# Kernel optimization log

Measured on AMD Instinct MI355X. Metric: run time of the kernel, lower is better.

## Reference

```python
import jax, jax.numpy as jnp
import numpy as np

NSIDE = 64
NLAT = 4 * NSIDE - 1        # 255 iso-latitude rings
NLON = 4 * NSIDE            # 256 = max pixels per ring
NPIX = 12 * NSIDE * NSIDE   # 49152 HEALPix pixels
LMAX = NLAT                 # 255
MMAX = NLON // 2 + 1        # 129
BATCH, CHAN = 8, 32


def _ring_geometry():
    # HEALPix ring scheme: ring r (0-based), 1-based i=r+1
    #  north cap i<nside: nph=4i, phi shift 0.5
    #  equatorial nside<=i<=3*nside: nph=4*nside, shift alternates {0,0.5}
    #  south cap: mirror of north cap
    nph = np.zeros(NLAT, np.int64)
    shift = np.zeros(NLAT, np.float64)
    for r in range(NLAT):
        i = r + 1
        if i < NSIDE:
            nph[r], shift[r] = 4 * i, 0.5
        elif i <= 3 * NSIDE:
            nph[r], shift[r] = 4 * NSIDE, 0.5 * ((i - NSIDE + 1) % 2)
        else:
            nph[r], shift[r] = 4 * (NLAT - r), 0.5
    offs = np.concatenate([[0], np.cumsum(nph)[:-1]])
    p = np.arange(NLON)
    mask = (p[None, :] < nph[:, None])                       # [nlat, nlon]
    idx = (offs[:, None] + p[None, :]) * mask                # padded -> 0
    phase = 2.0 * np.pi * (p[None, :] + shift[:, None]) / nph[:, None] * mask
    return idx.astype(np.int32), mask.astype(np.float32), phase.astype(np.float32)


def setup_inputs() -> dict:
    key = jax.random.key(0)
    k1, k2, k3 = jax.random.split(key, 3)
    idx, mask, phase = _ring_geometry()
    x = jax.random.normal(k1, (BATCH, CHAN, NPIX), jnp.float32)
    pct = jax.random.normal(k2, (MMAX, LMAX, NLAT), jnp.float32) * 0.1  # Legendre table stand-in
    w = jax.random.uniform(k3, (NLAT,), jnp.float32)                    # per-ring quadrature weights
    return {"x": x, "pct": pct, "w": w,
            "ring_index": jnp.asarray(idx),
            "ring_mask": jnp.asarray(mask),
            "phase": jnp.asarray(phase)}


def _healpix_rfft_real(x, ring_index, ring_mask, phase):
    # x: [..., npix] -> per-ring DFT coefficients as real pairs [..., nlat, mmax, 2]
    rings = x[..., ring_index] * ring_mask                 # [..., nlat, nlon]
    m = jnp.arange(MMAX, dtype=phase.dtype)
    ang = phase[:, :, None] * m                            # [nlat, nlon, mmax]
    fr = jnp.einsum('...kp,kpm->...km', rings, jnp.cos(ang))
    fi = -jnp.einsum('...kp,kpm->...km', rings, jnp.sin(ang))
    return jnp.stack([fr, fi], axis=-1)                    # n=2 is view_as_real axis


def reference(x, pct, w, ring_index, ring_mask, phase):
    # healpix ring rFFT, then Legendre contraction (einsum '...kmn,mlk->...lmn')
    f = _healpix_rfft_real(x, ring_index, ring_mask, phase)  # [..., nlat, mmax, 2]
    weights = pct * w                                        # [mmax, lmax, nlat]
    out = jnp.einsum('...kmn,mlk->...lmn', f, weights)       # [..., lmax, mmax, 2]
    return out
```

## Files before the change

kernel.cpp:

```cpp
#include <hip/hip_runtime.h>

#define NLAT 255
#define NLON 256
#define NPIX 49152
#define MMAX 129
#define MCS  258
#define NTBL 65
#define TROWS 264

typedef unsigned short ushort_t;
typedef __attribute__((ext_vector_type(8)))  short  bf16x8;
typedef __attribute__((ext_vector_type(4)))  short  short4v;
typedef __attribute__((ext_vector_type(16))) float  f32x16;
typedef __attribute__((ext_vector_type(4)))  float  float4v;

__device__ __forceinline__ ushort_t f2bf(float f) {
    union { float f; unsigned u; } v; v.f = f;
    unsigned r = v.u + 0x7FFFu + ((v.u >> 16) & 1u);
    return (ushort_t)(r >> 16);
}
__device__ __forceinline__ float bf2f(ushort_t h) {
    union { unsigned u; float f; } v; v.u = ((unsigned)h) << 16;
    return v.f;
}

__global__ __launch_bounds__(256) void prepK(const float* __restrict__ pct,
                                             const float* __restrict__ w,
                                             ushort_t* __restrict__ pctw) {
    const int m  = blockIdx.x;
    const int l0 = blockIdx.y * 32;
    const int t  = threadIdx.x;
    const float wk = (t < NLAT) ? w[t] : 0.f;
    for (int l = l0; l < l0 + 32; ++l) {
        float v = 0.f;
        if (l < NLAT && t < NLAT)
            v = pct[((size_t)m * NLAT + l) * NLAT + t] * wk;
        pctw[((size_t)m * 256 + l) * 256 + t] = f2bf(v);
    }
}

__global__ __launch_bounds__(256) void trigK(const float* __restrict__ phase,
                                             const float* __restrict__ mask,
                                             ushort_t* __restrict__ Ttab3) {
    const int tt  = blockIdx.x;
    const int mcs = blockIdx.y;
    const int p   = threadIdx.x;
    const int r   = (tt < 63) ? tt : (tt == 63 ? 63 : 64);
    float val = 0.f;
    if (mcs < MCS) {
        float ph = phase[r * NLON + p];
        float mk = mask[r * NLON + p];
        float fm = (float)(mcs >> 1);
        float s, c;
        __sincosf(ph * fm, &s, &c);
        val = (mcs & 1) ? (-s * mk) : (c * mk);
    }
    const int pcc = p >> 6, c = (p >> 3) & 7, j = p & 7;
    Ttab3[((((size_t)tt * 4 + pcc) * 8 + c) * TROWS + mcs) * 8 + j] = f2bf(val);
}

__global__ __launch_bounds__(256, 2) void stageA(const float* __restrict__ x,
                                                 const int* __restrict__ ring_index,
                                                 const ushort_t* __restrict__ Ttab3,
                                                 ushort_t* __restrict__ f1) {
    __shared__ __align__(16) ushort_t Rs[2][64 * 72];

    const int b0 = blockIdx.x * 64;
    const int r  = blockIdx.y;
    const int i1 = r + 1;
    const int nph = (i1 < 64) ? 4 * i1 : (i1 <= 192 ? 256 : 4 * (256 - i1));
    const int tbl = (i1 < 64) ? r : (i1 <= 192 ? (63 + (((i1 - 63) & 1) ^ 1)) : 254 - r);
    const int base = ring_index[r * NLON];
    const int nchunks = (nph + 63) >> 6;

    const int t    = threadIdx.x;
    const int lane = t & 63;
    const int wid  = t >> 6;
    const int wrow = wid >> 1, wcol = wid & 1;
    const int lg   = lane >> 5;
    const int lc   = lane & 31;

    f32x16 acc[5];
#pragma unroll
    for (int tau = 0; tau < 5; ++tau)
#pragma unroll
        for (int q = 0; q < 16; ++q) acc[tau][q] = 0.f;

    int trow[5];
#pragma unroll
    for (int tau = 0; tau < 5; ++tau) {
        int rr = tau * 64 + wcol * 32 + lc;
        trow[tau] = rr > (TROWS - 1) ? (TROWS - 1) : rr;
    }

    float4v rx[4];
    const int p0 = (t & 15) * 4;
    auto ldX = [&](int pc) {
        const bool ok = (pc + p0) < nph;
#pragma unroll
        for (int pass = 0; pass < 4; ++pass) {
            int bc = (t >> 4) + pass * 16;
            float4v v = {0.f, 0.f, 0.f, 0.f};
            if (ok) v = *(const float4v*)(x + (size_t)(b0 + bc) * NPIX + base + pc + p0);
            rx[pass] = v;
        }
    };
    auto stX = [&](ushort_t* dst) {
#pragma unroll
        for (int pass = 0; pass < 4; ++pass) {
            int bc = (t >> 4) + pass * 16;
            short4v h;
            h[0] = (short)f2bf(rx[pass][0]); h[1] = (short)f2bf(rx[pass][1]);
            h[2] = (short)f2bf(rx[pass][2]); h[3] = (short)f2bf(rx[pass][3]);
            *(short4v*)(dst + bc * 72 + p0) = h;
        }
    };

    ldX(0);
    stX(Rs[0]);
    __syncthreads();

    for (int c = 0; c < nchunks; ++c) {
        const int pc = c << 6;
        const bool more = (c + 1) < nchunks;
        const ushort_t* slab = Ttab3 + (size_t)(tbl * 4 + c) * (8 * TROWS * 8);

        bf16x8 bfr[4][5];
#pragma unroll
        for (int ks = 0; ks < 4; ++ks) {
            const ushort_t* bcol = slab + (size_t)(ks * 2 + lg) * (TROWS * 8);
#pragma unroll
            for (int tau = 0; tau < 5; ++tau)
                bfr[ks][tau] = *(const bf16x8*)(bcol + trow[tau] * 8);
        }
        if (more) ldX(pc + 64);

        const ushort_t* Rcur = Rs[c & 1];
#pragma unroll
        for (int ks = 0; ks < 4; ++ks) {
            bf16x8 a = *(const bf16x8*)(Rcur + (wrow * 32 + lc) * 72 + ks * 16 + lg * 8);
#pragma unroll
            for (int tau = 0; tau < 5; ++tau)
                acc[tau] = __builtin_amdgcn_mfma_f32_32x32x16_bf16(a, bfr[ks][tau], acc[tau], 0, 0, 0);
        }
        if (more) stX(Rs[(c + 1) & 1]);
        __syncthreads();
    }

    ushort_t* Olds = Rs[0];
#pragma unroll
    for (int tau = 0; tau < 5; ++tau) {
        __syncthreads();
        {
            const int mcsl = wcol * 32 + lc;
#pragma unroll
            for (int q = 0; q < 16; ++q) {
                int bcl = wrow * 32 + 4 * lg + (q & 3) + 8 * (q >> 2);
                Olds[mcsl * 72 + bcl] = f2bf(acc[tau][q]);
            }
        }
        __syncthreads();
        {
            int row = t >> 2;
            int mcs = tau * 64 + row;
            if (mcs < MCS) {
                int m = mcs >> 1, n = mcs & 1;
                size_t gbase = ((size_t)m * NLAT + r) * 512 + n * 256 + b0 + (t & 3) * 16;
#pragma unroll
                for (int j = 0; j < 2; ++j) {
                    bf16x8 v = *(const bf16x8*)(Olds + row * 72 + (t & 3) * 16 + j * 8);
                    *(bf16x8*)(f1 + gbase + j * 8) = v;
                }
            }
        }
    }
}

__global__ __launch_bounds__(256) void transK(const ushort_t* __restrict__ f1,
                                              ushort_t* __restrict__ f1t) {
    __shared__ __align__(16) ushort_t T[64][72];
    const int m  = blockIdx.x;
    const int k0 = blockIdx.y * 64;
    const int b0 = blockIdx.z * 64;
    const int t  = threadIdx.x;
#pragma unroll
    for (int it = 0; it < 2; ++it) {
        int id = t + it * 256;
        int kk = id >> 3, ch = id & 7;
        int k  = k0 + kk;
        bf16x8 v = {0,0,0,0,0,0,0,0};
        if (k < NLAT)
            v = *(const bf16x8*)(f1 + ((size_t)m * NLAT + k) * 512 + b0 + ch * 8);
        *(bf16x8*)(&T[kk][ch * 8]) = v;
    }
    __syncthreads();
#pragma unroll
    for (int it = 0; it < 2; ++it) {
        int id  = t + it * 256;
        int bb  = id & 63, ch8 = id >> 6;
        bf16x8 v;
#pragma unroll
        for (int j = 0; j < 8; ++j) v[j] = T[ch8 * 8 + j][bb];
        *(bf16x8*)(f1t + ((size_t)m * 512 + b0 + bb) * 256 + k0 + ch8 * 8) = v;
    }
}

__global__ __launch_bounds__(256, 2) void stageB(const ushort_t* __restrict__ f1t,
                                                 const ushort_t* __restrict__ pctw,
                                                 ushort_t* __restrict__ otmp) {
    __shared__ __align__(16) ushort_t SB[30720];
    ushort_t* As = SB;
    ushort_t* Ws = SB + 10240;
    ushort_t* Es = SB;

    const int id = blockIdx.x;
    const int m  = ((id >> 5) << 3) | (id & 7);
    if (m >= MMAX) return;
    const int sub = (id >> 3) & 3;
    const int b2t = sub * 128;

    const int t     = threadIdx.x;
    const int lane  = t & 63;
    const int wid   = t >> 6;
    const int wrow  = wid >> 1, wlcol = wid & 1;
    const int lg    = lane >> 5, lc = lane & 31;

    f32x16 acc[2][4];
#pragma unroll
    for (int i = 0; i < 2; ++i)
#pragma unroll
        for (int j = 0; j < 4; ++j)
#pragma unroll
            for (int q = 0; q < 16; ++q) acc[i][j][q] = 0.f;

    bf16x8 ra[2], rw[4];
    auto ldA = [&](int kc) {
#pragma unroll
        for (int pass = 0; pass < 2; ++pass) {
            int id2 = t + pass * 256;
            int row = id2 >> 2, ch = id2 & 3;
            ra[pass] = *(const bf16x8*)(f1t + ((size_t)m * 512 + b2t + row) * 256 + kc + ch * 8);
        }
    };
    auto ldW = [&](int kc) {
#pragma unroll
        for (int pass = 0; pass < 4; ++pass) {
            int id2 = t + pass * 256;
            int row = id2 >> 2, ch = id2 & 3;
            rw[pass] = *(const bf16x8*)(pctw + ((size_t)m * 256 + row) * 256 + kc + ch * 8);
        }
    };
    auto stA = [&](ushort_t* dst) {
#pragma unroll
        for (int pass = 0; pass < 2; ++pass) {
            int id2 = t + pass * 256;
            int row = id2 >> 2, ch = id2 & 3;
            *(bf16x8*)(dst + row * 40 + ch * 8) = ra[pass];
        }
    };
    auto stW = [&](ushort_t* dst) {
#pragma unroll
        for (int pass = 0; pass < 4; ++pass) {
            int id2 = t + pass * 256;
            int row = id2 >> 2, ch = id2 & 3;
            *(bf16x8*)(dst + row * 40 + ch * 8) = rw[pass];
        }
    };

    ldA(0); ldW(0);
    stA(As); stW(Ws);
    __syncthreads();
    int buf = 0;
    for (int kc = 0; kc < 256; kc += 32, buf ^= 1) {
        const bool more = (kc + 32) < 256;
        if (more) { ldA(kc + 32); ldW(kc + 32); }
        const ushort_t* A = As + buf * 5120;
        const ushort_t* W = Ws + buf * 10240;
#pragma unroll
        for (int ks = 0; ks < 2; ++ks) {
            const int ko = ks * 16 + lg * 8;
            bf16x8 a0 = *(const bf16x8*)(A + (wrow * 64 + lc) * 40 + ko);
            bf16x8 a1 = *(const bf16x8*)(A + (wrow * 64 + 32 + lc) * 40 + ko);
#pragma unroll
            for (int jj = 0; jj < 4; ++jj) {
                bf16x8 b = *(const bf16x8*)(W + (wlcol * 128 + jj * 32 + lc) * 40 + ko);
                acc[0][jj] = __builtin_amdgcn_mfma_f32_32x32x16_bf16(a0, b, acc[0][jj], 0, 0, 0);
                acc[1][jj] = __builtin_amdgcn_mfma_f32_32x32x16_bf16(a1, b, acc[1][jj], 0, 0, 0);
            }
        }
        if (more) { stA(As + (buf ^ 1) * 5120); stW(Ws + (buf ^ 1) * 10240); }
        __syncthreads();
    }

#pragma unroll
    for (int h = 0; h < 2; ++h) {
        if (h) __syncthreads();
        if (wlcol == h) {
#pragma unroll
            for (int i = 0; i < 2; ++i)
#pragma unroll
                for (int jj = 0; jj < 4; ++jj)
#pragma unroll
                    for (int q = 0; q < 16; ++q) {
                        int bl = wrow * 64 + i * 32 + 4 * lg + (q & 3) + 8 * (q >> 2);
                        Es[bl * 136 + jj * 32 + lc] = f2bf(acc[i][jj][q]);
                    }
        }
        __syncthreads();
#pragma unroll
        for (int it = 0; it < 8; ++it) {
            int id2 = t + it * 256;
            int row = id2 >> 4, ch = id2 & 15;
            bf16x8 v = *(const bf16x8*)(Es + row * 136 + ch * 8);
            *(bf16x8*)(otmp + (((size_t)m * 512 + b2t + row) << 8) + h * 128 + ch * 8) = v;
        }
    }
}

__global__ __launch_bounds__(256) void permuteK(const ushort_t* __restrict__ otmp,
                                                float* __restrict__ out) {
    __shared__ ushort_t L[MCS * 66];
    const int bc = blockIdx.x;
    const int l0 = blockIdx.y * 64;
    const int t  = threadIdx.x;
    const int ll = t & 63;
    const int l  = l0 + ll;
#pragma unroll 4
    for (int it = 0; it < 65; ++it) {
        int mn = (t >> 6) + it * 4;
        if (mn < MCS) {
            int mm = mn >> 1, n = mn & 1;
            ushort_t v = 0;
            if (l < NLAT)
                v = otmp[(((size_t)mm * 512 + n * 256 + bc) << 8) + l];
            L[mn * 66 + ll] = v;
        }
    }
    __syncthreads();
    for (int ll2 = 0; ll2 < 64; ++ll2) {
        int lo = l0 + ll2;
        if (lo >= NLAT) break;
        size_t rowb = ((size_t)bc * NLAT + lo) * MCS;
        out[rowb + t] = bf2f(L[t * 66 + ll2]);
        if (t < 2)
            out[rowb + 256 + t] = bf2f(L[(256 + t) * 66 + ll2]);
    }
}

extern "C" void kernel_launch(void* const* d_in, const int* in_sizes, int n_in,
                              void* d_out, int out_size, void* d_ws, size_t ws_size,
                              hipStream_t stream) {
    const float* x          = (const float*)d_in[0];
    const float* pct        = (const float*)d_in[1];
    const float* w          = (const float*)d_in[2];
    const int*   ring_index = (const int*)d_in[3];
    const float* ring_mask  = (const float*)d_in[4];
    const float* phase      = (const float*)d_in[5];
    float* out = (float*)d_out;

    char* wsb = (char*)d_ws;
    char* ob  = (char*)d_out;
    ushort_t* otmp  = (ushort_t*)wsb;
    ushort_t* f1    = (ushort_t*)(wsb + 33552384);
    ushort_t* f1t   = (ushort_t*)ob;
    ushort_t* pctw  = (ushort_t*)(ob + 33816576);
    ushort_t* Ttab3 = (ushort_t*)(ob + 50724864);

    prepK   <<<dim3(MMAX, 8),     256, 0, stream>>>(pct, w, pctw);
    trigK   <<<dim3(NTBL, TROWS), 256, 0, stream>>>(phase, ring_mask, Ttab3);
    stageA  <<<dim3(4, NLAT),     256, 0, stream>>>(x, ring_index, Ttab3, f1);
    transK  <<<dim3(MMAX, 4, 8),  256, 0, stream>>>(f1, f1t);
    stageB  <<<dim3(544),         256, 0, stream>>>(f1t, pctw, otmp);
    permuteK<<<dim3(256, 4),      256, 0, stream>>>(otmp, out);
}
```

Before: 125.4 us.

## Pre-swizzle stageB operands into MFMA fragment layout and drop LDS staging

```diff
diff --git a/kernel.cpp b/kernel.cpp
--- a/kernel.cpp
+++ b/kernel.cpp
@@ -26,16 +26,17 @@
 
 __global__ __launch_bounds__(256) void prepK(const float* __restrict__ pct,
                                              const float* __restrict__ w,
-                                             ushort_t* __restrict__ pctw) {
+                                             ushort_t* __restrict__ pctwF) {
     const int m  = blockIdx.x;
     const int l0 = blockIdx.y * 32;
     const int t  = threadIdx.x;
     const float wk = (t < NLAT) ? w[t] : 0.f;
+    const int kg = t >> 3, j = t & 7;
     for (int l = l0; l < l0 + 32; ++l) {
         float v = 0.f;
         if (l < NLAT && t < NLAT)
             v = pct[((size_t)m * NLAT + l) * NLAT + t] * wk;
-        pctw[((size_t)m * 256 + l) * 256 + t] = f2bf(v);
+        pctwF[(((size_t)m * 32 + kg) * 256 + l) * 8 + j] = f2bf(v);
     }
 }
 
@@ -177,7 +178,7 @@
 }
 
 __global__ __launch_bounds__(256) void transK(const ushort_t* __restrict__ f1,
-                                              ushort_t* __restrict__ f1t) {
+                                              ushort_t* __restrict__ f1tF) {
     __shared__ __align__(16) ushort_t T[64][72];
     const int m  = blockIdx.x;
     const int k0 = blockIdx.y * 64;
@@ -201,23 +202,17 @@
         bf16x8 v;
 #pragma unroll
         for (int j = 0; j < 8; ++j) v[j] = T[ch8 * 8 + j][bb];
-        *(bf16x8*)(f1t + ((size_t)m * 512 + b0 + bb) * 256 + k0 + ch8 * 8) = v;
-    }
-}
-
-__global__ __launch_bounds__(256, 2) void stageB(const ushort_t* __restrict__ f1t,
-                                                 const ushort_t* __restrict__ pctw,
+        *(bf16x8*)(f1tF + (((size_t)m * 32 + (k0 >> 3) + ch8) * 512 + b0 + bb) * 8) = v;
+    }
+}
+
+__global__ __launch_bounds__(256, 2) void stageB(const ushort_t* __restrict__ f1tF,
+                                                 const ushort_t* __restrict__ pctwF,
                                                  ushort_t* __restrict__ otmp) {
-    __shared__ __align__(16) ushort_t SB[30720];
-    ushort_t* As = SB;
-    ushort_t* Ws = SB + 10240;
-    ushort_t* Es = SB;
-
-    const int id = blockIdx.x;
-    const int m  = ((id >> 5) << 3) | (id & 7);
-    if (m >= MMAX) return;
-    const int sub = (id >> 3) & 3;
-    const int b2t = sub * 128;
+    __shared__ __align__(16) ushort_t Es[128 * 136];
+
+    const int m   = blockIdx.x >> 2;
+    const int b2t = (blockIdx.x & 3) * 128;
 
     const int t     = threadIdx.x;
     const int lane  = t & 63;
@@ -233,63 +228,36 @@
 #pragma unroll
             for (int q = 0; q < 16; ++q) acc[i][j][q] = 0.f;
 
-    bf16x8 ra[2], rw[4];
-    auto ldA = [&](int kc) {
-#pragma unroll
-        for (int pass = 0; pass < 2; ++pass) {
-            int id2 = t + pass * 256;
-            int row = id2 >> 2, ch = id2 & 3;
-            ra[pass] = *(const bf16x8*)(f1t + ((size_t)m * 512 + b2t + row) * 256 + kc + ch * 8);
-        }
+    const ushort_t* aBase = f1tF  + (((size_t)m * 32 + lg) * 512 + b2t + wrow * 64 + lc) * 8;
+    const ushort_t* bBase = pctwF + (((size_t)m * 32 + lg) * 256 + wlcol * 128 + lc) * 8;
+
+    bf16x8 fa0[2], fb0[4], fa1[2], fb1[4];
+    auto ldf = [&](int ksm, bf16x8* fa, bf16x8* fb) {
+        const size_t ao = (size_t)ksm * 8192;
+        const size_t bo = (size_t)ksm * 4096;
+#pragma unroll
+        for (int i = 0; i < 2; ++i)
+            fa[i] = *(const bf16x8*)(aBase + ao + i * 256);
+#pragma unroll
+        for (int jj = 0; jj < 4; ++jj)
+            fb[jj] = *(const bf16x8*)(bBase + bo + jj * 256);
     };
-    auto ldW = [&](int kc) {
-#pragma unroll
-        for (int pass = 0; pass < 4; ++pass) {
-            int id2 = t + pass * 256;
-            int row = id2 >> 2, ch = id2 & 3;
-            rw[pass] = *(const bf16x8*)(pctw + ((size_t)m * 256 + row) * 256 + kc + ch * 8);
+    auto mm = [&](const bf16x8* fa, const bf16x8* fb) {
+#pragma unroll
+        for (int jj = 0; jj < 4; ++jj) {
+            acc[0][jj] = __builtin_amdgcn_mfma_f32_32x32x16_bf16(fa[0], fb[jj], acc[0][jj], 0, 0, 0);
+            acc[1][jj] = __builtin_amdgcn_mfma_f32_32x32x16_bf16(fa[1], fb[jj], acc[1][jj], 0, 0, 0);
         }
     };
-    auto stA = [&](ushort_t* dst) {
-#pragma unroll
-        for (int pass = 0; pass < 2; ++pass) {
-            int id2 = t + pass * 256;
-            int row = id2 >> 2, ch = id2 & 3;
-            *(bf16x8*)(dst + row * 40 + ch * 8) = ra[pass];
-        }
-    };
-    auto stW = [&](ushort_t* dst) {
-#pragma unroll
-        for (int pass = 0; pass < 4; ++pass) {
-            int id2 = t + pass * 256;
-            int row = id2 >> 2, ch = id2 & 3;
-            *(bf16x8*)(dst + row * 40 + ch * 8) = rw[pass];
-        }
-    };
-
-    ldA(0); ldW(0);
-    stA(As); stW(Ws);
-    __syncthreads();
-    int buf = 0;
-    for (int kc = 0; kc < 256; kc += 32, buf ^= 1) {
-        const bool more = (kc + 32) < 256;
-        if (more) { ldA(kc + 32); ldW(kc + 32); }
-        const ushort_t* A = As + buf * 5120;
-        const ushort_t* W = Ws + buf * 10240;
-#pragma unroll
-        for (int ks = 0; ks < 2; ++ks) {
-            const int ko = ks * 16 + lg * 8;
-            bf16x8 a0 = *(const bf16x8*)(A + (wrow * 64 + lc) * 40 + ko);
-            bf16x8 a1 = *(const bf16x8*)(A + (wrow * 64 + 32 + lc) * 40 + ko);
-#pragma unroll
-            for (int jj = 0; jj < 4; ++jj) {
-                bf16x8 b = *(const bf16x8*)(W + (wlcol * 128 + jj * 32 + lc) * 40 + ko);
-                acc[0][jj] = __builtin_amdgcn_mfma_f32_32x32x16_bf16(a0, b, acc[0][jj], 0, 0, 0);
-                acc[1][jj] = __builtin_amdgcn_mfma_f32_32x32x16_bf16(a1, b, acc[1][jj], 0, 0, 0);
-            }
-        }
-        if (more) { stA(As + (buf ^ 1) * 5120); stW(Ws + (buf ^ 1) * 10240); }
-        __syncthreads();
+
+    ldf(0, fa0, fb0);
+    ldf(1, fa1, fb1);
+#pragma unroll
+    for (int ksm = 0; ksm < 16; ksm += 2) {
+        mm(fa0, fb0);
+        if (ksm + 2 < 16) ldf(ksm + 2, fa0, fb0);
+        mm(fa1, fb1);
+        if (ksm + 3 < 16) ldf(ksm + 3, fa1, fb1);
     }
 
 #pragma unroll
@@ -362,14 +330,14 @@
     char* ob  = (char*)d_out;
     ushort_t* otmp  = (ushort_t*)wsb;
     ushort_t* f1    = (ushort_t*)(wsb + 33552384);
-    ushort_t* f1t   = (ushort_t*)ob;
-    ushort_t* pctw  = (ushort_t*)(ob + 33816576);
+    ushort_t* f1tF  = (ushort_t*)ob;
+    ushort_t* pctwF = (ushort_t*)(ob + 33816576);
     ushort_t* Ttab3 = (ushort_t*)(ob + 50724864);
 
-    prepK   <<<dim3(MMAX, 8),     256, 0, stream>>>(pct, w, pctw);
+    prepK   <<<dim3(MMAX, 8),     256, 0, stream>>>(pct, w, pctwF);
     trigK   <<<dim3(NTBL, TROWS), 256, 0, stream>>>(phase, ring_mask, Ttab3);
     stageA  <<<dim3(4, NLAT),     256, 0, stream>>>(x, ring_index, Ttab3, f1);
-    transK  <<<dim3(MMAX, 4, 8),  256, 0, stream>>>(f1, f1t);
-    stageB  <<<dim3(544),         256, 0, stream>>>(f1t, pctw, otmp);
+    transK  <<<dim3(MMAX, 4, 8),  256, 0, stream>>>(f1, f1tF);
+    stageB  <<<dim3(4 * MMAX),    256, 0, stream>>>(f1tF, pctwF, otmp);
     permuteK<<<dim3(256, 4),      256, 0, stream>>>(otmp, out);
 }
```

After: 128.8 us. +2.7%, slower.
